# Optimization experiments

Hardware: AMD Instinct MI355X
Metric: run time of the kernel (lower is better)

The kernel has to match this reference:

```python
import jax, jax.numpy as jnp
import numpy as np

N_POINTS = 1048576
FEATURES = 64
RES = 256


def setup_inputs() -> dict:
    key = jax.random.key(0)
    k1, k2, k3, k4 = jax.random.split(key, 4)
    x = jax.random.uniform(k1, (N_POINTS, 3), jnp.float32, -1.0, 1.0)
    plane_xy = jax.random.normal(k2, (1, FEATURES, RES, RES), jnp.float32)
    plane_xz = jax.random.normal(k3, (1, FEATURES, RES, RES), jnp.float32)
    plane_yz = jax.random.normal(k4, (1, FEATURES, RES, RES), jnp.float32)
    pose = jnp.zeros((1,), jnp.float32)
    person_id = 0
    return {"x": x, "plane_xy": plane_xy, "plane_xz": plane_xz,
            "plane_yz": plane_yz, "pose": pose, "person_id": person_id}


def _grid_sample_points(plane, uv):
    """Bilinear sample. plane: [1,C,IH,IW], uv: [N,2] in [-1,1]. Returns [N,C].
    Matches the hand-rolled torch grid_sample (align_corners=True semantics,
    corner indices clamped, weights computed from unclamped floor coords)."""
    C, IH, IW = plane.shape[1], plane.shape[2], plane.shape[3]
    ix = (uv[:, 0] + 1.0) * 0.5 * (IW - 1)
    iy = (uv[:, 1] + 1.0) * 0.5 * (IH - 1)
    fx0 = jnp.floor(ix)
    fy0 = jnp.floor(iy)
    # bilinear weights (differentiable w.r.t. ix, iy)
    w_nw = (fx0 + 1.0 - ix) * (fy0 + 1.0 - iy)
    w_ne = (ix - fx0) * (fy0 + 1.0 - iy)
    w_sw = (fx0 + 1.0 - ix) * (iy - fy0)
    w_se = (ix - fx0) * (iy - fy0)
    # clamped integer corner indices (non-differentiable, as in torch no_grad)
    x0 = jnp.clip(fx0, 0, IW - 1).astype(jnp.int32)
    x1 = jnp.clip(fx0 + 1.0, 0, IW - 1).astype(jnp.int32)
    y0 = jnp.clip(fy0, 0, IH - 1).astype(jnp.int32)
    y1 = jnp.clip(fy0 + 1.0, 0, IH - 1).astype(jnp.int32)
    pf = plane.reshape(C, IH * IW)  # [C, IH*IW]
    v_nw = pf[:, y0 * IW + x0]  # [C, N]
    v_ne = pf[:, y0 * IW + x1]
    v_sw = pf[:, y1 * IW + x0]
    v_se = pf[:, y1 * IW + x1]
    out = v_nw * w_nw + v_ne * w_ne + v_sw * w_sw + v_se * w_se  # [C, N]
    return out.T  # [N, C]


def reference(x, plane_xy, plane_xz, plane_yz, pose, person_id):
    # person_id selects the (single) person's planes; pose is unused upstream.
    feat_xy = _grid_sample_points(plane_xy, x[:, [0, 1]])
    feat_xz = _grid_sample_points(plane_xz, x[:, [0, 2]])
    feat_yz = _grid_sample_points(plane_yz, x[:, [1, 2]])
    feat = (feat_xy + feat_xz + feat_yz) / 3.0  # [N, FEATURES]
    return feat
```

## Files before the change

### kernel.cpp

```cpp
#include <hip/hip_runtime.h>

#define N_POINTS 1048576
#define FEAT 64
#define RES 256
#define PLANE_ELEMS (FEAT * RES * RES)

#define BUCKET_G 32
#define NBUCKET (BUCKET_G * BUCKET_G * BUCKET_G)

#define SAMPLE_BLOCKS (N_POINTS / 32)
#define SAMPLE_CPX (SAMPLE_BLOCKS / 8)

#define TRANSPOSE_BLOCKS (3 * (RES * RES / 64))
#define COUNT_BLOCKS (N_POINTS / 256)
#define PREP_BLOCKS (TRANSPOSE_BLOCKS + COUNT_BLOCKS)

typedef unsigned short ushort_t;
typedef float v4f __attribute__((ext_vector_type(4)));
typedef _Float16 half8 __attribute__((ext_vector_type(8)));

__device__ __forceinline__ ushort_t f2h(float f) {
  _Float16 h = (_Float16)f;
  return __builtin_bit_cast(unsigned short, h);
}

__device__ __forceinline__ unsigned part1by2(unsigned v) {
  v &= 0x3FFu;
  v = (v | (v << 16)) & 0x030000FFu;
  v = (v | (v << 8)) & 0x0300F00Fu;
  v = (v | (v << 4)) & 0x030C30C3u;
  v = (v | (v << 2)) & 0x09249249u;
  return v;
}

__device__ __forceinline__ unsigned morton_bucket(float px, float py, float pz) {
  int bx = (int)((px + 1.0f) * (0.5f * BUCKET_G));
  int by = (int)((py + 1.0f) * (0.5f * BUCKET_G));
  int bz = (int)((pz + 1.0f) * (0.5f * BUCKET_G));
  bx = min(max(bx, 0), BUCKET_G - 1);
  by = min(max(by, 0), BUCKET_G - 1);
  bz = min(max(bz, 0), BUCKET_G - 1);
  return part1by2((unsigned)bx) | (part1by2((unsigned)by) << 1) |
         (part1by2((unsigned)bz) << 2);
}

__global__ __launch_bounds__(256) void prep_transpose_count(
    const float* __restrict__ pxy, const float* __restrict__ pxz,
    const float* __restrict__ pyz, ushort_t* __restrict__ dst,
    const float* __restrict__ x, unsigned* __restrict__ hist) {
  const int b = blockIdx.x;
  const int tid = threadIdx.x;
  if (b >= TRANSPOSE_BLOCKS) {
    int n = (b - TRANSPOSE_BLOCKS) * 256 + tid;
    float px = x[n * 3 + 0];
    float py = x[n * 3 + 1];
    float pz = x[n * 3 + 2];
    atomicAdd(&hist[morton_bucket(px, py, pz)], 1u);
    return;
  }
  __shared__ ushort_t tile[64][72];
  const int plane = b >> 10;
  const int p0 = (b & 1023) * 64;
  const float* src = (plane == 0) ? pxy : ((plane == 1) ? pxz : pyz);
  ushort_t* out = dst + (size_t)plane * PLANE_ELEMS;
#pragma unroll
  for (int k = 0; k < 4; ++k) {
    int c = (tid >> 4) + k * 16;
    int pp = (tid & 15) * 4;
    v4f v = __builtin_nontemporal_load(
        (const v4f*)(src + (size_t)c * (RES * RES) + p0 + pp));
    tile[pp + 0][c] = f2h(v.x);
    tile[pp + 1][c] = f2h(v.y);
    tile[pp + 2][c] = f2h(v.z);
    tile[pp + 3][c] = f2h(v.w);
  }
  __syncthreads();
#pragma unroll
  for (int k = 0; k < 2; ++k) {
    int idx = k * 256 + tid;
    int pp = idx >> 3;
    int c8 = (idx & 7) * 8;
    uint4 v = *(const uint4*)&tile[pp][c8];
    *(uint4*)(out + (size_t)(p0 + pp) * FEAT + c8) = v;
  }
}

__global__ __launch_bounds__(1024) void scan_hist(
    const unsigned* __restrict__ hist, unsigned* __restrict__ cursor) {
  __shared__ unsigned part[1024];
  const int tid = threadIdx.x;
  unsigned local[32];
  unsigned s = 0;
#pragma unroll
  for (int i = 0; i < 32; ++i) {
    local[i] = s;
    s += hist[tid * 32 + i];
  }
  part[tid] = s;
  __syncthreads();
  for (int off = 1; off < 1024; off <<= 1) {
    unsigned add = (tid >= off) ? part[tid - off] : 0u;
    __syncthreads();
    part[tid] += add;
    __syncthreads();
  }
  unsigned base = (tid == 0) ? 0u : part[tid - 1];
#pragma unroll
  for (int i = 0; i < 32; ++i) cursor[tid * 32 + i] = base + local[i];
}

__global__ __launch_bounds__(256) void bucket_scatter(
    const float* __restrict__ x, unsigned* __restrict__ cursor,
    float4* __restrict__ xs) {
  int n = blockIdx.x * 256 + threadIdx.x;
  float px = x[n * 3 + 0];
  float py = x[n * 3 + 1];
  float pz = x[n * 3 + 2];
  unsigned b = morton_bucket(px, py, pz);
  unsigned pos = atomicAdd(&cursor[b], 1u);
  xs[pos] = make_float4(px, py, pz, __uint_as_float((unsigned)n));
}

struct PlaneRef {
  const half8 *p00, *p01, *p10, *p11;
  float w00, w01, w10, w11;
};

__device__ __forceinline__ PlaneRef plane_ref(const ushort_t* __restrict__ tp,
                                              float u, float v, int c8) {
  float ix = fmaf(u, 0.5f * (float)(RES - 1), 0.5f * (float)(RES - 1));
  float iy = fmaf(v, 0.5f * (float)(RES - 1), 0.5f * (float)(RES - 1));
  float fx0 = floorf(ix), fy0 = floorf(iy);
  float wx1 = ix - fx0, wy1 = iy - fy0;
  float wx0 = fx0 + 1.0f - ix, wy0 = fy0 + 1.0f - iy;
  int x0 = min(max((int)fx0, 0), RES - 1);
  int y0 = min(max((int)fy0, 0), RES - 1);
  int x1 = min(max((int)fx0 + 1, 0), RES - 1);
  int y1 = min(max((int)fy0 + 1, 0), RES - 1);
  PlaneRef r;
  r.p00 = (const half8*)(tp + (size_t)(y0 * RES + x0) * FEAT + c8);
  r.p01 = (const half8*)(tp + (size_t)(y0 * RES + x1) * FEAT + c8);
  r.p10 = (const half8*)(tp + (size_t)(y1 * RES + x0) * FEAT + c8);
  r.p11 = (const half8*)(tp + (size_t)(y1 * RES + x1) * FEAT + c8);
  r.w00 = wx0 * wy0;
  r.w01 = wx1 * wy0;
  r.w10 = wx0 * wy1;
  r.w11 = wx1 * wy1;
  return r;
}

__device__ __forceinline__ void fma_mix8(half8 v, float w, float* acc) {
#pragma unroll
  for (int j = 0; j < 8; ++j) acc[j] = fmaf((float)v[j], w, acc[j]);
}

__device__ __forceinline__ void sample3(const ushort_t* __restrict__ tps,
                                        float px, float py, float pz, int c8,
                                        float* acc) {
  PlaneRef A = plane_ref(tps, px, py, c8);
  PlaneRef B = plane_ref(tps + PLANE_ELEMS, px, pz, c8);
  PlaneRef C = plane_ref(tps + 2 * PLANE_ELEMS, py, pz, c8);

  const half8 a00 = *A.p00, a01 = *A.p01, a10 = *A.p10, a11 = *A.p11;
  const half8 b00 = *B.p00, b01 = *B.p01, b10 = *B.p10, b11 = *B.p11;
  const half8 c00 = *C.p00, c01 = *C.p01, c10 = *C.p10, c11 = *C.p11;

  fma_mix8(a00, A.w00, acc);
  fma_mix8(a01, A.w01, acc);
  fma_mix8(a10, A.w10, acc);
  fma_mix8(a11, A.w11, acc);
  fma_mix8(b00, B.w00, acc);
  fma_mix8(b01, B.w01, acc);
  fma_mix8(b10, B.w10, acc);
  fma_mix8(b11, B.w11, acc);
  fma_mix8(c00, C.w00, acc);
  fma_mix8(c01, C.w01, acc);
  fma_mix8(c10, C.w10, acc);
  fma_mix8(c11, C.w11, acc);
}

__global__ __launch_bounds__(256) void triplane_sample_sorted(
    const float4* __restrict__ xs, const ushort_t* __restrict__ tps,
    float* __restrict__ out) {
  int bid = blockIdx.x;
  int swz = (bid & 7) * SAMPLE_CPX + (bid >> 3);
  int p = swz * 32 + (threadIdx.x >> 3);
  int c8 = (threadIdx.x & 7) << 3;

  v4f pt = __builtin_nontemporal_load((const v4f*)xs + p);
  unsigned n = __float_as_uint(pt.w);

  float acc[8] = {0.f, 0.f, 0.f, 0.f, 0.f, 0.f, 0.f, 0.f};
  sample3(tps, pt.x, pt.y, pt.z, c8, acc);

  const float s = 1.0f / 3.0f;
  v4f lo = {acc[0] * s, acc[1] * s, acc[2] * s, acc[3] * s};
  v4f hi = {acc[4] * s, acc[5] * s, acc[6] * s, acc[7] * s};
  float* o = out + (size_t)n * FEAT + c8;
  __builtin_nontemporal_store(lo, (v4f*)o);
  __builtin_nontemporal_store(hi, (v4f*)(o + 4));
}

__global__ __launch_bounds__(256) void transpose_only(
    const float* __restrict__ pxy, const float* __restrict__ pxz,
    const float* __restrict__ pyz, ushort_t* __restrict__ dst) {
  __shared__ ushort_t tile[64][72];
  const int plane = blockIdx.y;
  const float* src = (plane == 0) ? pxy : ((plane == 1) ? pxz : pyz);
  ushort_t* out = dst + (size_t)plane * PLANE_ELEMS;
  const int p0 = blockIdx.x * 64;
  const int tid = threadIdx.x;
#pragma unroll
  for (int k = 0; k < 4; ++k) {
    int c = (tid >> 4) + k * 16;
    int pp = (tid & 15) * 4;
    v4f v = *(const v4f*)(src + (size_t)c * (RES * RES) + p0 + pp);
    tile[pp + 0][c] = f2h(v.x);
    tile[pp + 1][c] = f2h(v.y);
    tile[pp + 2][c] = f2h(v.z);
    tile[pp + 3][c] = f2h(v.w);
  }
  __syncthreads();
#pragma unroll
  for (int k = 0; k < 2; ++k) {
    int idx = k * 256 + tid;
    int pp = idx >> 3;
    int c8 = (idx & 7) * 8;
    uint4 v = *(const uint4*)&tile[pp][c8];
    *(uint4*)(out + (size_t)(p0 + pp) * FEAT + c8) = v;
  }
}

__global__ __launch_bounds__(256) void triplane_sample_f16(
    const float* __restrict__ x, const ushort_t* __restrict__ tps,
    float* __restrict__ out) {
  int t = blockIdx.x * 256 + threadIdx.x;
  int n = t >> 3;
  int c8 = (t & 7) << 3;
  float px = __builtin_nontemporal_load(x + n * 3 + 0);
  float py = __builtin_nontemporal_load(x + n * 3 + 1);
  float pz = __builtin_nontemporal_load(x + n * 3 + 2);
  float acc[8] = {0.f, 0.f, 0.f, 0.f, 0.f, 0.f, 0.f, 0.f};
  sample3(tps, px, py, pz, c8, acc);
  const float s = 1.0f / 3.0f;
  v4f lo = {acc[0] * s, acc[1] * s, acc[2] * s, acc[3] * s};
  v4f hi = {acc[4] * s, acc[5] * s, acc[6] * s, acc[7] * s};
  float* o = out + (size_t)n * FEAT + c8;
  __builtin_nontemporal_store(lo, (v4f*)o);
  __builtin_nontemporal_store(hi, (v4f*)(o + 4));
}

__device__ __forceinline__ float sample_one(const float* __restrict__ pc,
                                            float u, float v) {
  float ix = (u + 1.0f) * 0.5f * (float)(RES - 1);
  float iy = (v + 1.0f) * 0.5f * (float)(RES - 1);
  float fx0 = floorf(ix), fy0 = floorf(iy);
  float wx1 = ix - fx0, wy1 = iy - fy0;
  float wx0 = fx0 + 1.0f - ix, wy0 = fy0 + 1.0f - iy;
  int x0 = min(max((int)fx0, 0), RES - 1);
  int y0 = min(max((int)fy0, 0), RES - 1);
  int x1 = min(max((int)fx0 + 1, 0), RES - 1);
  int y1 = min(max((int)fy0 + 1, 0), RES - 1);
  return pc[y0 * RES + x0] * (wx0 * wy0) + pc[y0 * RES + x1] * (wx1 * wy0) +
         pc[y1 * RES + x0] * (wx0 * wy1) + pc[y1 * RES + x1] * (wx1 * wy1);
}

__global__ __launch_bounds__(256) void triplane_direct(
    const float* __restrict__ x, const float* __restrict__ pxy,
    const float* __restrict__ pxz, const float* __restrict__ pyz,
    float* __restrict__ out) {
  int t = blockIdx.x * 256 + threadIdx.x;
  int n = t >> 6;
  int c = t & 63;
  float px = x[n * 3 + 0];
  float py = x[n * 3 + 1];
  float pz = x[n * 3 + 2];
  const size_t cs = (size_t)c * (RES * RES);
  float acc = sample_one(pxy + cs, px, py) + sample_one(pxz + cs, px, pz) +
              sample_one(pyz + cs, py, pz);
  out[(size_t)n * FEAT + c] = acc * (1.0f / 3.0f);
}

extern "C" void kernel_launch(void* const* d_in, const int* in_sizes, int n_in,
                              void* d_out, int out_size, void* d_ws,
                              size_t ws_size, hipStream_t stream) {
  const float* x   = (const float*)d_in[0];
  const float* pxy = (const float*)d_in[1];
  const float* pxz = (const float*)d_in[2];
  const float* pyz = (const float*)d_in[3];
  float* out = (float*)d_out;

  const size_t tps_bytes = (size_t)3 * PLANE_ELEMS * sizeof(ushort_t);
  const size_t xs_bytes  = (size_t)N_POINTS * sizeof(float4);
  const size_t cnt_bytes = (size_t)NBUCKET * sizeof(unsigned);
  const size_t need_sorted = tps_bytes + xs_bytes + 2 * cnt_bytes;

  if (ws_size >= need_sorted) {
    ushort_t* tps    = (ushort_t*)d_ws;
    float4* xs       = (float4*)((char*)d_ws + tps_bytes);
    unsigned* cursor = (unsigned*)((char*)d_ws + tps_bytes + xs_bytes);
    unsigned* hist   = cursor + NBUCKET;

    (void)hipMemsetAsync(hist, 0, cnt_bytes, stream);
    prep_transpose_count<<<PREP_BLOCKS, 256, 0, stream>>>(pxy, pxz, pyz, tps,
                                                          x, hist);
    scan_hist<<<1, 1024, 0, stream>>>(hist, cursor);
    bucket_scatter<<<N_POINTS / 256, 256, 0, stream>>>(x, cursor, xs);
    triplane_sample_sorted<<<SAMPLE_BLOCKS, 256, 0, stream>>>(xs, tps, out);
  } else if (ws_size >= tps_bytes) {
    ushort_t* tps = (ushort_t*)d_ws;
    dim3 tgrid(RES * RES / 64, 3);
    transpose_only<<<tgrid, 256, 0, stream>>>(pxy, pxz, pyz, tps);
    triplane_sample_f16<<<(N_POINTS * 8) / 256, 256, 0, stream>>>(x, tps, out);
  } else {
    triplane_direct<<<(N_POINTS * 64) / 256, 256, 0, stream>>>(x, pxy, pxz,
                                                               pyz, out);
  }
}
```

Before: 469.6 us.

## Store transposed planes in 8x8 spatial tiles and vectorize histogram scan

```diff
diff --git a/kernel.cpp b/kernel.cpp
--- a/kernel.cpp
+++ b/kernel.cpp
@@ -22,6 +22,11 @@
 __device__ __forceinline__ ushort_t f2h(float f) {
   _Float16 h = (_Float16)f;
   return __builtin_bit_cast(unsigned short, h);
+}
+
+__device__ __forceinline__ int tiled_elem(int y, int x, int c8) {
+  return (((y >> 3) << 5 | (x >> 3)) << 12) + (((y & 7) << 3 | (x & 7)) << 6) +
+         c8;
 }
 
 __device__ __forceinline__ unsigned part1by2(unsigned v) {
@@ -61,6 +66,8 @@
   __shared__ ushort_t tile[64][72];
   const int plane = b >> 10;
   const int p0 = (b & 1023) * 64;
+  const int y = p0 >> 8;
+  const int xb = p0 & 255;
   const float* src = (plane == 0) ? pxy : ((plane == 1) ? pxz : pyz);
   ushort_t* out = dst + (size_t)plane * PLANE_ELEMS;
 #pragma unroll
@@ -81,20 +88,31 @@
     int pp = idx >> 3;
     int c8 = (idx & 7) * 8;
     uint4 v = *(const uint4*)&tile[pp][c8];
-    *(uint4*)(out + (size_t)(p0 + pp) * FEAT + c8) = v;
+    *(uint4*)(out + tiled_elem(y, xb + pp, c8)) = v;
   }
 }
 
 __global__ __launch_bounds__(1024) void scan_hist(
-    const unsigned* __restrict__ hist, unsigned* __restrict__ cursor) {
+    const uint4* __restrict__ hist4, unsigned* __restrict__ cursor) {
   __shared__ unsigned part[1024];
   const int tid = threadIdx.x;
+  uint4 h[8];
+#pragma unroll
+  for (int i = 0; i < 8; ++i) h[i] = hist4[tid * 8 + i];
+  unsigned vals[32];
+#pragma unroll
+  for (int i = 0; i < 8; ++i) {
+    vals[i * 4 + 0] = h[i].x;
+    vals[i * 4 + 1] = h[i].y;
+    vals[i * 4 + 2] = h[i].z;
+    vals[i * 4 + 3] = h[i].w;
+  }
   unsigned local[32];
   unsigned s = 0;
 #pragma unroll
   for (int i = 0; i < 32; ++i) {
     local[i] = s;
-    s += hist[tid * 32 + i];
+    s += vals[i];
   }
   part[tid] = s;
   __syncthreads();
@@ -105,8 +123,16 @@
     __syncthreads();
   }
   unsigned base = (tid == 0) ? 0u : part[tid - 1];
-#pragma unroll
-  for (int i = 0; i < 32; ++i) cursor[tid * 32 + i] = base + local[i];
+  uint4* cur4 = (uint4*)cursor;
+#pragma unroll
+  for (int i = 0; i < 8; ++i) {
+    uint4 o;
+    o.x = base + local[i * 4 + 0];
+    o.y = base + local[i * 4 + 1];
+    o.z = base + local[i * 4 + 2];
+    o.w = base + local[i * 4 + 3];
+    cur4[tid * 8 + i] = o;
+  }
 }
 
 __global__ __launch_bounds__(256) void bucket_scatter(
@@ -138,10 +164,10 @@
   int x1 = min(max((int)fx0 + 1, 0), RES - 1);
   int y1 = min(max((int)fy0 + 1, 0), RES - 1);
   PlaneRef r;
-  r.p00 = (const half8*)(tp + (size_t)(y0 * RES + x0) * FEAT + c8);
-  r.p01 = (const half8*)(tp + (size_t)(y0 * RES + x1) * FEAT + c8);
-  r.p10 = (const half8*)(tp + (size_t)(y1 * RES + x0) * FEAT + c8);
-  r.p11 = (const half8*)(tp + (size_t)(y1 * RES + x1) * FEAT + c8);
+  r.p00 = (const half8*)(tp + tiled_elem(y0, x0, c8));
+  r.p01 = (const half8*)(tp + tiled_elem(y0, x1, c8));
+  r.p10 = (const half8*)(tp + tiled_elem(y1, x0, c8));
+  r.p11 = (const half8*)(tp + tiled_elem(y1, x1, c8));
   r.w00 = wx0 * wy0;
   r.w01 = wx1 * wy0;
   r.w10 = wx0 * wy1;
@@ -209,6 +235,8 @@
   const float* src = (plane == 0) ? pxy : ((plane == 1) ? pxz : pyz);
   ushort_t* out = dst + (size_t)plane * PLANE_ELEMS;
   const int p0 = blockIdx.x * 64;
+  const int y = p0 >> 8;
+  const int xb = p0 & 255;
   const int tid = threadIdx.x;
 #pragma unroll
   for (int k = 0; k < 4; ++k) {
@@ -227,7 +255,7 @@
     int pp = idx >> 3;
     int c8 = (idx & 7) * 8;
     uint4 v = *(const uint4*)&tile[pp][c8];
-    *(uint4*)(out + (size_t)(p0 + pp) * FEAT + c8) = v;
+    *(uint4*)(out + tiled_elem(y, xb + pp, c8)) = v;
   }
 }
 
@@ -304,7 +332,7 @@
     (void)hipMemsetAsync(hist, 0, cnt_bytes, stream);
     prep_transpose_count<<<PREP_BLOCKS, 256, 0, stream>>>(pxy, pxz, pyz, tps,
                                                           x, hist);
-    scan_hist<<<1, 1024, 0, stream>>>(hist, cursor);
+    scan_hist<<<1, 1024, 0, stream>>>((const uint4*)hist, cursor);
     bucket_scatter<<<N_POINTS / 256, 256, 0, stream>>>(x, cursor, xs);
     triplane_sample_sorted<<<SAMPLE_BLOCKS, 256, 0, stream>>>(xs, tps, out);
   } else if (ws_size >= tps_bytes) {
```

Measured after the change: 462.5 us. No clear change (-1.5%).
